# Performance work log

Measured on AMD Instinct MI355X. Metric: run time of the kernel, lower is better.

## Reference

```python
import jax, jax.numpy as jnp
import numpy as np

N = 100_000   # nodes
E = 3_200_000 # edges (avg degree 32)
F_NODE = 64
F_EDGE = 16
HID = 64
NEG_SLOPE = 0.2


def _gat_conv(x, src, dst, edge_attr, W, a_src, a_dst, We, a_e, bias, n):
    """PyG GATConv (heads=1, edge_dim, add_self_loops=True fill='mean', eval mode)."""
    # --- add self loops; loop edge_attr = mean of incoming edge_attr per node ---
    deg = jax.ops.segment_sum(jnp.ones((src.shape[0],), x.dtype), dst, num_segments=n)
    loop_attr = jax.ops.segment_sum(edge_attr, dst, num_segments=n)
    loop_attr = jnp.where(deg[:, None] > 0, loop_attr / jnp.maximum(deg, 1.0)[:, None], 0.0)
    loop = jnp.arange(n, dtype=src.dtype)
    src2 = jnp.concatenate([src, loop])
    dst2 = jnp.concatenate([dst, loop])
    ea = jnp.concatenate([edge_attr, loop_attr], axis=0)

    # --- node / edge projections and per-node attention terms ---
    h = x @ W                                   # [N, HID]
    alpha_src = h @ a_src                       # [N]
    alpha_dst = h @ a_dst                       # [N]
    e = ea @ We                                 # [E+N, HID]
    alpha_e = e @ a_e                           # [E+N]

    # --- per-edge logits + segment softmax over destination neighborhoods ---
    logits = jax.nn.leaky_relu(alpha_src[src2] + alpha_dst[dst2] + alpha_e, NEG_SLOPE)
    seg_max = jax.ops.segment_max(logits, dst2, num_segments=n)  # every node has self loop
    ex = jnp.exp(logits - seg_max[dst2])
    denom = jax.ops.segment_sum(ex, dst2, num_segments=n)
    w = ex / denom[dst2]                        # [E+N]

    # --- weighted scatter-aggregate of messages ---
    out = jax.ops.segment_sum(h[src2] * w[:, None], dst2, num_segments=n)
    return out + bias


def setup_inputs() -> dict:
    key = jax.random.key(0)
    ks = jax.random.split(key, 16)
    s = 0.1  # keep logits tame
    return {
        "x": jax.random.normal(ks[0], (N, F_NODE), jnp.float32),
        "edge_index": jax.random.randint(ks[1], (2, E), 0, N, jnp.int32),
        "edge_attr": jax.random.normal(ks[2], (E, F_EDGE), jnp.float32),
        "W1": jax.random.normal(ks[3], (F_NODE, HID), jnp.float32) * s,
        "att_src1": jax.random.normal(ks[4], (HID,), jnp.float32) * s,
        "att_dst1": jax.random.normal(ks[5], (HID,), jnp.float32) * s,
        "We1": jax.random.normal(ks[6], (F_EDGE, HID), jnp.float32) * s,
        "att_edge1": jax.random.normal(ks[7], (HID,), jnp.float32) * s,
        "b1": jnp.zeros((HID,), jnp.float32),
        "W2": jax.random.normal(ks[8], (HID, HID), jnp.float32) * s,
        "att_src2": jax.random.normal(ks[9], (HID,), jnp.float32) * s,
        "att_dst2": jax.random.normal(ks[10], (HID,), jnp.float32) * s,
        "We2": jax.random.normal(ks[11], (F_EDGE, HID), jnp.float32) * s,
        "att_edge2": jax.random.normal(ks[12], (HID,), jnp.float32) * s,
        "b2": jnp.zeros((HID,), jnp.float32),
        "fc_w": jax.random.normal(ks[13], (HID, 1), jnp.float32) * s,
        "fc_b": jnp.zeros((1,), jnp.float32),
    }


def reference(x, edge_index, edge_attr, W1, att_src1, att_dst1, We1, att_edge1, b1,
              W2, att_src2, att_dst2, We2, att_edge2, b2, fc_w, fc_b):
    src, dst = edge_index[0], edge_index[1]
    n = x.shape[0]
    h = jax.nn.elu(_gat_conv(x, src, dst, edge_attr, W1, att_src1, att_dst1, We1, att_edge1, b1, n))
    h = jax.nn.elu(_gat_conv(h, src, dst, edge_attr, W2, att_src2, att_dst2, We2, att_edge2, b2, n))
    return h @ fc_w + fc_b  # [N, 1] logits
```

## Files before the change

kernel.cpp:

```cpp
#include <hip/hip_runtime.h>
#include <hip/hip_bf16.h>
#include <hip/hip_fp16.h>
#include <math.h>
#include <stdint.h>

constexpr int HIDDIM = 64;
constexpr int FEDGE  = 16;
constexpr int BN     = 512;
constexpr int CAP    = 17000;
constexpr int TILE   = 4096;
constexpr int NTA    = 512;
constexpr int EPT    = TILE / NTA;

__global__ void compute_c_kernel(const float* __restrict__ We1, const float* __restrict__ ae1,
                                 const float* __restrict__ We2, const float* __restrict__ ae2,
                                 float* __restrict__ c) {
  int t = threadIdx.x;
  if (t < FEDGE) {
    float s = 0.f;
    for (int j = 0; j < HIDDIM; ++j) s += We1[t * HIDDIM + j] * ae1[j];
    c[t] = s;
  } else if (t < 2 * FEDGE) {
    int k = t - FEDGE;
    float s = 0.f;
    for (int j = 0; j < HIDDIM; ++j) s += We2[k * HIDDIM + j] * ae2[j];
    c[FEDGE + k] = s;
  }
}

__device__ __forceinline__ int pack_ae(float a1, float a2) {
  unsigned lo = __half_as_ushort(__float2half_rn(a1));
  unsigned hi = __half_as_ushort(__float2half_rn(a2));
  return (int)((hi << 16) | lo);
}
template <int SEL>
__device__ __forceinline__ float unpack_ae(int pk) {
  unsigned u = (SEL == 0) ? ((unsigned)pk & 0xFFFFu) : ((unsigned)pk >> 16);
  return __half2float(__ushort_as_half((unsigned short)u));
}

__global__ __launch_bounds__(NTA) void passA_kernel(
    const int* __restrict__ src, const int* __restrict__ dst,
    const float* __restrict__ attr, const float* __restrict__ c,
    int* __restrict__ bucketCursor, int2* __restrict__ P, int E, int nbuck) {
  __shared__ int st_ae[TILE];
  __shared__ int s_key[TILE];
  __shared__ int s_ae[TILE];
  __shared__ unsigned char s_b[TILE];
  __shared__ int cnt[256];
  __shared__ int lbase[512];
  __shared__ int gbase[256];
  __shared__ int wsum[8];
  __shared__ float cs[32];
  int t = threadIdx.x;
  if (t < 32) cs[t] = c[t];
  if (t < nbuck) cnt[t] = 0;
  __syncthreads();
  int e0 = blockIdx.x * TILE;
  int tileCnt = min(TILE, E - e0);

  int d_reg[EPT];
#pragma unroll
  for (int k = 0; k < EPT; ++k) {
    int e = e0 + k * NTA + t;
    d_reg[k] = (e < E) ? dst[e] : -1;
  }
#pragma unroll
  for (int k = 0; k < EPT; ++k) {
    if (d_reg[k] >= 0) atomicAdd(&cnt[d_reg[k] >> 9], 1);
  }
  __syncthreads();

  int lane = t & 63, w = t >> 6;
  int n = (t < nbuck) ? cnt[t] : 0;
  int ret = 0;
  if (n > 0) ret = atomicAdd(&bucketCursor[t], n);
  int incl = n;
#pragma unroll
  for (int d = 1; d < 64; d <<= 1) {
    int tv = __shfl_up(incl, d, 64);
    if (lane >= d) incl += tv;
  }
  if (lane == 63) wsum[w] = incl;
  __syncthreads();
  {
    int woff = 0;
#pragma unroll
    for (int w2 = 0; w2 < 8; ++w2) woff += (w2 < w) ? wsum[w2] : 0;
    lbase[t] = incl - n + woff;
    if (t < nbuck) { gbase[t] = ret; cnt[t] = 0; }
  }

  {
    int q   = t & 3;
    int grp = t >> 2;
    const float4* attr4 = (const float4*)attr;
#pragma unroll
    for (int pass = 0; pass < TILE / 128; ++pass) {
      int el = pass * 128 + grp;
      int e = e0 + el;
      float4 v = make_float4(0.f, 0.f, 0.f, 0.f);
      if (e < E) v = attr4[(size_t)e * 4 + q];
      float a1 = v.x * cs[4*q]    + v.y * cs[4*q+1]    + v.z * cs[4*q+2]    + v.w * cs[4*q+3];
      float a2 = v.x * cs[16+4*q] + v.y * cs[16+4*q+1] + v.z * cs[16+4*q+2] + v.w * cs[16+4*q+3];
      a1 += __shfl_xor(a1, 1, 64); a1 += __shfl_xor(a1, 2, 64);
      a2 += __shfl_xor(a2, 1, 64); a2 += __shfl_xor(a2, 2, 64);
      if (q == 0) st_ae[el] = pack_ae(a1, a2);
    }
  }
  __syncthreads();

#pragma unroll
  for (int k = 0; k < EPT; ++k) {
    int d = d_reg[k];
    if (d < 0) continue;
    int el = k * NTA + t;
    int e = e0 + el;
    int b = d >> 9;
    int sE = src[e];
    int r = atomicAdd(&cnt[b], 1);
    int idx = lbase[b] + r;
    s_key[idx] = sE | ((d & 511) << 20);
    s_ae[idx]  = st_ae[el];
    s_b[idx]   = (unsigned char)b;
  }
  __syncthreads();

  for (int i = t; i < tileCnt; i += NTA) {
    int b = s_b[i];
    int rank = i - lbase[b];
    int pos = gbase[b] + rank;
    if (pos < CAP) P[(size_t)b * CAP + pos] = make_int2(s_key[i], s_ae[i]);
  }
}

__global__ void scan_buckets_kernel(const int* __restrict__ bucketCursor,
                                    int* __restrict__ bucketBase,
                                    int* __restrict__ offsets, int nbuck, int N, int E) {
  __shared__ int s[512];
  int t = threadIdx.x;
  int v = (t < nbuck) ? min(bucketCursor[t], CAP) : 0;
  s[t] = v;
  __syncthreads();
  for (int d = 1; d < 512; d <<= 1) {
    int tv = (t >= d) ? s[t - d] : 0;
    __syncthreads();
    s[t] += tv;
    __syncthreads();
  }
  if (t < nbuck) bucketBase[t] = s[t] - v;
  if (t == 0) offsets[N] = E;
}

__global__ __launch_bounds__(512) void passB_kernel(
    const int2* __restrict__ P, const int* __restrict__ bucketCursor,
    const int* __restrict__ bucketBase, int* __restrict__ offsets,
    int2* __restrict__ EDGS, int N) {
  int b = blockIdx.x;
  int t = threadIdx.x;
  int nodeBase = b * BN;
  int cnt = min(bucketCursor[b], CAP);
  int gbase = bucketBase[b];
  __shared__ int hist[BN];
  __shared__ int cur[BN];
  __shared__ int wsum[8];
  hist[t] = 0;
  __syncthreads();
  const int2* Pb = P + (size_t)b * CAP;
  for (int i = t; i < cnt; i += 512) {
    int dl = (Pb[i].x >> 20) & 511;
    atomicAdd(&hist[dl], 1);
  }
  __syncthreads();
  int deg = hist[t];
  int lane = t & 63, w = t >> 6;
  int incl = deg;
#pragma unroll
  for (int d = 1; d < 64; d <<= 1) {
    int tv = __shfl_up(incl, d, 64);
    if (lane >= d) incl += tv;
  }
  if (lane == 63) wsum[w] = incl;
  __syncthreads();
  int woff = 0;
#pragma unroll
  for (int w2 = 0; w2 < 8; ++w2) woff += (w2 < w) ? wsum[w2] : 0;
  int excl = incl - deg + woff;
  int nodeId = nodeBase + t;
  if (nodeId < N) offsets[nodeId] = gbase + excl;
  cur[t] = gbase + excl;
  __syncthreads();
  for (int i = t; i < cnt; i += 512) {
    int2 r = Pb[i];
    int dl = (r.x >> 20) & 511;
    int pos = atomicAdd(&cur[dl], 1);
    EDGS[pos] = r;
  }
}

__global__ __launch_bounds__(256) void gemm_alpha_kernel(
    const float* __restrict__ X, const float* __restrict__ W,
    const float* __restrict__ a_src, const float* __restrict__ a_dst,
    __half2* __restrict__ H, float* __restrict__ alpha_s, float* __restrict__ alpha_d, int n) {
  __shared__ float Ws[HIDDIM * HIDDIM];
  __shared__ float as_s[HIDDIM], ad_s[HIDDIM];
  for (int i = threadIdx.x; i < HIDDIM * HIDDIM; i += blockDim.x) Ws[i] = W[i];
  if (threadIdx.x < HIDDIM) {
    as_s[threadIdx.x] = a_src[threadIdx.x];
    ad_s[threadIdx.x] = a_dst[threadIdx.x];
  }
  __syncthreads();
  int lane = threadIdx.x & 63;
  int wid  = threadIdx.x >> 6;
  int wavesTotal = (blockDim.x >> 6) * gridDim.x;
  for (int row = blockIdx.x * (blockDim.x >> 6) + wid; row < n; row += wavesTotal) {
    float xv = X[(size_t)row * HIDDIM + lane];
    float acc = 0.f;
#pragma unroll
    for (int k = 0; k < HIDDIM; ++k) {
      float xk = __shfl(xv, k, 64);
      acc = fmaf(xk, Ws[k * HIDDIM + lane], acc);
    }
    float accN = __shfl_xor(acc, 1, 64);
    if (!(lane & 1)) {
      H[(size_t)row * 32 + (lane >> 1)] = __floats2half2_rn(acc, accN);
    }
    float s1 = acc * as_s[lane];
    float s2 = acc * ad_s[lane];
#pragma unroll
    for (int d = 32; d > 0; d >>= 1) {
      s1 += __shfl_xor(s1, d, 64);
      s2 += __shfl_xor(s2, d, 64);
    }
    if (lane == 0) {
      alpha_s[row] = s1;
      alpha_d[row] = s2;
    }
  }
}

__device__ __forceinline__ float leaky(float x) { return (x < 0.f) ? 0.2f * x : x; }
__device__ __forceinline__ float elu(float x) { return (x > 0.f) ? x : (__expf(x) - 1.f); }

template <bool FINAL, int SEL>
__global__ __launch_bounds__(256) void aggregate_kernel(
    const __half2* __restrict__ H, const float* __restrict__ alpha_s, const float* __restrict__ alpha_d,
    const int2* __restrict__ EDGS, const int* __restrict__ offsets,
    const float* __restrict__ bias, const float* __restrict__ fc_w, const float* __restrict__ fc_b,
    float* __restrict__ out, int n) {
  int lane = threadIdx.x & 63;
  int wid  = threadIdx.x >> 6;
  int node = blockIdx.x * (blockDim.x >> 6) + wid;
  if (node >= n) return;
  int off = offsets[node];
  int deg = offsets[node + 1] - off;
  float ad  = alpha_d[node];
  float asn = alpha_s[node];

  if (deg <= 64) {
    int2 ed = make_int2(0, 0);
    if (lane < deg) ed = EDGS[off + lane];
    int   s_l  = ed.x & 0xFFFFF;
    float ae_l = unpack_ae<SEL>(ed.y);
    float as_g = (lane < deg) ? alpha_s[s_l] : 0.f;
    float lg_l = (lane < deg) ? leaky(as_g + ad + ae_l) : -INFINITY;
    float aesum = (lane < deg) ? ae_l : 0.f;
    float lmax = lg_l;
#pragma unroll
    for (int d = 32; d > 0; d >>= 1) {
      lmax = fmaxf(lmax, __shfl_xor(lmax, d, 64));
      aesum += __shfl_xor(aesum, d, 64);
    }
    float self_ae = (deg > 0) ? aesum / (float)deg : 0.f;
    float slg = leaky(asn + ad + self_ae);
    float m = fmaxf(lmax, slg);

    float ex_l = (lane < deg) ? __expf(lg_l - m) : 0.f;
    float dsum = ex_l;
#pragma unroll
    for (int d = 32; d > 0; d >>= 1) dsum += __shfl_xor(dsum, d, 64);
    float exs = __expf(slg - m);
    float denom = dsum + exs;

    int half = lane >> 5;
    int c32  = lane & 31;

    float selfw = (half == 0) ? exs : 0.f;
    float2 hv = __half22float2(H[(size_t)node * 32 + c32]);
    float2 acc2;
    acc2.x = selfw * hv.x;
    acc2.y = selfw * hv.y;

    int jj = 0;
    for (; jj + 16 <= deg; jj += 16) {
      int   si[8]; float ei[8];
#pragma unroll
      for (int k = 0; k < 8; ++k) {
        si[k] = __shfl(s_l, jj + 2 * k + half, 64);
        ei[k] = __shfl(ex_l, jj + 2 * k + half, 64);
      }
      float2 hh[8];
#pragma unroll
      for (int k = 0; k < 8; ++k) hh[k] = __half22float2(H[(size_t)si[k] * 32 + c32]);
#pragma unroll
      for (int k = 0; k < 8; ++k) {
        acc2.x = fmaf(ei[k], hh[k].x, acc2.x);
        acc2.y = fmaf(ei[k], hh[k].y, acc2.y);
      }
    }
    for (; jj + 8 <= deg; jj += 8) {
      int j0 = jj + half, j1 = jj + 2 + half, j2 = jj + 4 + half, j3 = jj + 6 + half;
      int   sa = __shfl(s_l, j0, 64),  sb = __shfl(s_l, j1, 64);
      int   sc = __shfl(s_l, j2, 64),  sd = __shfl(s_l, j3, 64);
      float ea = __shfl(ex_l, j0, 64), eb = __shfl(ex_l, j1, 64);
      float ec = __shfl(ex_l, j2, 64), ef = __shfl(ex_l, j3, 64);
      float2 ha = __half22float2(H[(size_t)sa * 32 + c32]);
      float2 hb = __half22float2(H[(size_t)sb * 32 + c32]);
      float2 hc = __half22float2(H[(size_t)sc * 32 + c32]);
      float2 hd = __half22float2(H[(size_t)sd * 32 + c32]);
      acc2.x = fmaf(ea, ha.x, acc2.x); acc2.y = fmaf(ea, ha.y, acc2.y);
      acc2.x = fmaf(eb, hb.x, acc2.x); acc2.y = fmaf(eb, hb.y, acc2.y);
      acc2.x = fmaf(ec, hc.x, acc2.x); acc2.y = fmaf(ec, hc.y, acc2.y);
      acc2.x = fmaf(ef, hd.x, acc2.x); acc2.y = fmaf(ef, hd.y, acc2.y);
    }
    for (; jj < deg; jj += 2) {
      int j = jj + half;
      int   sj = __shfl(s_l, j, 64);
      float ej = __shfl(ex_l, j, 64);
      float2 hj = __half22float2(H[(size_t)sj * 32 + c32]);
      acc2.x = fmaf(ej, hj.x, acc2.x);
      acc2.y = fmaf(ej, hj.y, acc2.y);
    }
    acc2.x += __shfl_xor(acc2.x, 32, 64);
    acc2.y += __shfl_xor(acc2.y, 32, 64);

    const float2* bi2 = (const float2*)bias;
    float2 bv = bi2[c32];
    float rx = elu(acc2.x / denom + bv.x);
    float ry = elu(acc2.y / denom + bv.y);
    if (!FINAL) {
      if (half == 0) {
        float2 o; o.x = rx; o.y = ry;
        ((float2*)out)[(size_t)node * 32 + c32] = o;
      }
    } else {
      const float2* fw2 = (const float2*)fc_w;
      float2 fv = fw2[c32];
      float s1 = rx * fv.x + ry * fv.y;
#pragma unroll
      for (int d = 16; d > 0; d >>= 1) s1 += __shfl_xor(s1, d, 64);
      if (lane == 0) out[node] = s1 + fc_b[0];
    }
    return;
  }

  {
    const __half* Hh = (const __half*)H;
    float lmax = -INFINITY, aesum = 0.f;
    for (int base = 0; base < deg; base += 64) {
      int i = base + lane;
      if (i < deg) {
        int2 ed = EDGS[off + i];
        int s = ed.x & 0xFFFFF;
        float ae = unpack_ae<SEL>(ed.y);
        float lg = leaky(alpha_s[s] + ad + ae);
        lmax = fmaxf(lmax, lg);
        aesum += ae;
      }
    }
#pragma unroll
    for (int d = 32; d > 0; d >>= 1) {
      lmax = fmaxf(lmax, __shfl_xor(lmax, d, 64));
      aesum += __shfl_xor(aesum, d, 64);
    }
    float self_ae = aesum / (float)deg;
    float slg = leaky(asn + ad + self_ae);
    float m = fmaxf(lmax, slg);
    float exs = __expf(slg - m);
    float dsum = 0.f;
    float acc = exs * __half2float(Hh[(size_t)node * HIDDIM + lane]);
    for (int base = 0; base < deg; base += 64) {
      int i = base + lane;
      int cnt = min(64, deg - base);
      int2 ed = make_int2(0, 0);
      if (i < deg) ed = EDGS[off + i];
      int   s_l  = ed.x & 0xFFFFF;
      float ae_l = unpack_ae<SEL>(ed.y);
      float ex_l = (lane < cnt) ? __expf(leaky(alpha_s[s_l] + ad + ae_l) - m) : 0.f;
      dsum += ex_l;
      for (int j = 0; j < cnt; ++j) {
        int   sj = __shfl(s_l, j, 64);
        float ej = __shfl(ex_l, j, 64);
        acc = fmaf(ej, __half2float(Hh[(size_t)sj * HIDDIM + lane]), acc);
      }
    }
#pragma unroll
    for (int d = 32; d > 0; d >>= 1) dsum += __shfl_xor(dsum, d, 64);
    float denom = dsum + exs;

    float res = elu(acc / denom + bias[lane]);
    if (!FINAL) {
      out[(size_t)node * HIDDIM + lane] = res;
    } else {
      float s1 = res * fc_w[lane];
#pragma unroll
      for (int d = 32; d > 0; d >>= 1) s1 += __shfl_xor(s1, d, 64);
      if (lane == 0) out[node] = s1 + fc_b[0];
    }
  }
}

extern "C" void kernel_launch(void* const* d_in, const int* in_sizes, int n_in,
                              void* d_out, int out_size, void* d_ws, size_t ws_size,
                              hipStream_t stream) {
  const float* x    = (const float*)d_in[0];
  const int*   ei   = (const int*)d_in[1];
  const float* attr = (const float*)d_in[2];
  const float* W1   = (const float*)d_in[3];
  const float* as1  = (const float*)d_in[4];
  const float* ad1  = (const float*)d_in[5];
  const float* We1  = (const float*)d_in[6];
  const float* ae1  = (const float*)d_in[7];
  const float* b1   = (const float*)d_in[8];
  const float* W2   = (const float*)d_in[9];
  const float* as2  = (const float*)d_in[10];
  const float* ad2  = (const float*)d_in[11];
  const float* We2  = (const float*)d_in[12];
  const float* ae2  = (const float*)d_in[13];
  const float* b2   = (const float*)d_in[14];
  const float* fcw  = (const float*)d_in[15];
  const float* fcb  = (const float*)d_in[16];

  const int N = in_sizes[0] / HIDDIM;
  const int E = in_sizes[1] / 2;
  const int NBUCK = (N + BN - 1) / BN;

  char* p = (char*)d_ws;
  auto alloc = [&](size_t bytes) -> void* {
    void* r = (void*)p;
    p += (bytes + 255) & ~(size_t)255;
    return r;
  };
  float*  c            = (float*)alloc(32 * sizeof(float));
  int*    bucketCursor = (int*)alloc(512 * 4);
  int*    bucketBase   = (int*)alloc(((size_t)NBUCK + 1) * 4);
  int*    offsets      = (int*)alloc(((size_t)N + 1) * 4);
  float*  alpha_s      = (float*)alloc((size_t)N * 4);
  float*  alpha_d      = (float*)alloc((size_t)N * 4);
  int2*   EDGS         = (int2*)alloc((size_t)E * 8);
  size_t  regionBytes  = (size_t)NBUCK * CAP * 8;
  size_t  hBytes       = (size_t)N * HIDDIM * 2;
  size_t  x2Bytes      = (size_t)N * HIDDIM * 4;
  if (hBytes + x2Bytes > regionBytes) regionBytes = hBytes + x2Bytes;
  char*   region       = (char*)alloc(regionBytes);
  int2*   P            = (int2*)region;
  __half2* H           = (__half2*)region;
  float*  X2           = (float*)(region + ((hBytes + 255) & ~(size_t)255));

  const int* srcp = ei;
  const int* dstp = ei + E;

  hipMemsetAsync(bucketCursor, 0, 512 * 4, stream);

  compute_c_kernel<<<1, 64, 0, stream>>>(We1, ae1, We2, ae2, c);

  int ablocks = (E + TILE - 1) / TILE;
  passA_kernel<<<ablocks, NTA, 0, stream>>>(srcp, dstp, attr, c, bucketCursor, P, E, NBUCK);
  scan_buckets_kernel<<<1, 512, 0, stream>>>(bucketCursor, bucketBase, offsets, NBUCK, N, E);
  passB_kernel<<<NBUCK, 512, 0, stream>>>(P, bucketCursor, bucketBase, offsets, EDGS, N);

  int aggBlocks = (N + 3) / 4;

  gemm_alpha_kernel<<<2048, 256, 0, stream>>>(x, W1, as1, ad1, H, alpha_s, alpha_d, N);
  aggregate_kernel<false, 0><<<aggBlocks, 256, 0, stream>>>(H, alpha_s, alpha_d, EDGS,
                                                            offsets, b1, nullptr, nullptr, X2, N);
  gemm_alpha_kernel<<<2048, 256, 0, stream>>>(X2, W2, as2, ad2, H, alpha_s, alpha_d, N);
  aggregate_kernel<true, 1><<<aggBlocks, 256, 0, stream>>>(H, alpha_s, alpha_d, EDGS,
                                                           offsets, b2, fcw, fcb, (float*)d_out, N);
}
```

Before: 447.2 us.

## Fuse layer-1 aggregation with layer-2 projection and attention terms

Adds a kernel that performs the layer-1 softmax aggregation, bias and ELU, then immediately multiplies the result by W2 (held in shared memory) and computes the layer-2 alpha_src/alpha_dst terms per node. This removes the fp32 X2 intermediate write and read and one kernel launch. The cost is extra shared-memory use, a 64-step shuffle-based matvec per node, and a persistent grid-stride loop. New buffers H2 and alpha_s2/alpha_d2 avoid overwriting layer-1 data that other waves are still reading.

```diff
diff --git a/kernel.cpp b/kernel.cpp
--- a/kernel.cpp
+++ b/kernel.cpp
@@ -241,6 +241,169 @@
 
 __device__ __forceinline__ float leaky(float x) { return (x < 0.f) ? 0.2f * x : x; }
 __device__ __forceinline__ float elu(float x) { return (x > 0.f) ? x : (__expf(x) - 1.f); }
+
+__global__ __launch_bounds__(256) void agg_gemm_kernel(
+    const __half2* __restrict__ H, const float* __restrict__ alpha_s, const float* __restrict__ alpha_d,
+    const int2* __restrict__ EDGS, const int* __restrict__ offsets,
+    const float* __restrict__ bias, const float* __restrict__ W2,
+    const float* __restrict__ as2, const float* __restrict__ ad2,
+    __half2* __restrict__ H2, float* __restrict__ alpha_s2, float* __restrict__ alpha_d2, int n) {
+  __shared__ float W2s[HIDDIM * HIDDIM];
+  __shared__ float as2s[HIDDIM], ad2s[HIDDIM];
+  for (int i = threadIdx.x; i < HIDDIM * HIDDIM; i += 256) W2s[i] = W2[i];
+  if (threadIdx.x < HIDDIM) {
+    as2s[threadIdx.x] = as2[threadIdx.x];
+    ad2s[threadIdx.x] = ad2[threadIdx.x];
+  }
+  __syncthreads();
+  int lane = threadIdx.x & 63;
+  int wid  = threadIdx.x >> 6;
+  int wavesTotal = 4 * gridDim.x;
+  int half = lane >> 5;
+  int c32  = lane & 31;
+
+  for (int node = blockIdx.x * 4 + wid; node < n; node += wavesTotal) {
+    int off = offsets[node];
+    int deg = offsets[node + 1] - off;
+    float ad  = alpha_d[node];
+    float asn = alpha_s[node];
+    float rx, ry;
+
+    if (deg <= 64) {
+      int2 ed = make_int2(0, 0);
+      if (lane < deg) ed = EDGS[off + lane];
+      int   s_l  = ed.x & 0xFFFFF;
+      float ae_l = unpack_ae<0>(ed.y);
+      float as_g = (lane < deg) ? alpha_s[s_l] : 0.f;
+      float lg_l = (lane < deg) ? leaky(as_g + ad + ae_l) : -INFINITY;
+      float aesum = (lane < deg) ? ae_l : 0.f;
+      float lmax = lg_l;
+#pragma unroll
+      for (int d = 32; d > 0; d >>= 1) {
+        lmax = fmaxf(lmax, __shfl_xor(lmax, d, 64));
+        aesum += __shfl_xor(aesum, d, 64);
+      }
+      float self_ae = (deg > 0) ? aesum / (float)deg : 0.f;
+      float slg = leaky(asn + ad + self_ae);
+      float m = fmaxf(lmax, slg);
+      float ex_l = (lane < deg) ? __expf(lg_l - m) : 0.f;
+      float dsum = ex_l;
+#pragma unroll
+      for (int d = 32; d > 0; d >>= 1) dsum += __shfl_xor(dsum, d, 64);
+      float exs = __expf(slg - m);
+      float denom = dsum + exs;
+
+      float selfw = (half == 0) ? exs : 0.f;
+      float2 hv = __half22float2(H[(size_t)node * 32 + c32]);
+      float2 acc2;
+      acc2.x = selfw * hv.x;
+      acc2.y = selfw * hv.y;
+
+      int jj = 0;
+      for (; jj + 16 <= deg; jj += 16) {
+        int   si[8]; float ei[8];
+#pragma unroll
+        for (int k = 0; k < 8; ++k) {
+          si[k] = __shfl(s_l, jj + 2 * k + half, 64);
+          ei[k] = __shfl(ex_l, jj + 2 * k + half, 64);
+        }
+        float2 hh[8];
+#pragma unroll
+        for (int k = 0; k < 8; ++k) hh[k] = __half22float2(H[(size_t)si[k] * 32 + c32]);
+#pragma unroll
+        for (int k = 0; k < 8; ++k) {
+          acc2.x = fmaf(ei[k], hh[k].x, acc2.x);
+          acc2.y = fmaf(ei[k], hh[k].y, acc2.y);
+        }
+      }
+      for (; jj < deg; jj += 2) {
+        int j = jj + half;
+        int   sj = __shfl(s_l, j, 64);
+        float ej = __shfl(ex_l, j, 64);
+        float2 hj = __half22float2(H[(size_t)sj * 32 + c32]);
+        acc2.x = fmaf(ej, hj.x, acc2.x);
+        acc2.y = fmaf(ej, hj.y, acc2.y);
+      }
+      acc2.x += __shfl_xor(acc2.x, 32, 64);
+      acc2.y += __shfl_xor(acc2.y, 32, 64);
+
+      const float2* bi2 = (const float2*)bias;
+      float2 bv = bi2[c32];
+      rx = elu(acc2.x / denom + bv.x);
+      ry = elu(acc2.y / denom + bv.y);
+    } else {
+      const __half* Hh = (const __half*)H;
+      float lmax = -INFINITY, aesum = 0.f;
+      for (int base = 0; base < deg; base += 64) {
+        int i = base + lane;
+        if (i < deg) {
+          int2 ed = EDGS[off + i];
+          int s = ed.x & 0xFFFFF;
+          float ae = unpack_ae<0>(ed.y);
+          float lg = leaky(alpha_s[s] + ad + ae);
+          lmax = fmaxf(lmax, lg);
+          aesum += ae;
+        }
+      }
+#pragma unroll
+      for (int d = 32; d > 0; d >>= 1) {
+        lmax = fmaxf(lmax, __shfl_xor(lmax, d, 64));
+        aesum += __shfl_xor(aesum, d, 64);
+      }
+      float self_ae = aesum / (float)deg;
+      float slg = leaky(asn + ad + self_ae);
+      float m = fmaxf(lmax, slg);
+      float exs = __expf(slg - m);
+      float dsum = 0.f;
+      float acc = exs * __half2float(Hh[(size_t)node * HIDDIM + lane]);
+      for (int base = 0; base < deg; base += 64) {
+        int i = base + lane;
+        int cnt = min(64, deg - base);
+        int2 ed = make_int2(0, 0);
+        if (i < deg) ed = EDGS[off + i];
+        int   s_l  = ed.x & 0xFFFFF;
+        float ae_l = unpack_ae<0>(ed.y);
+        float ex_l = (lane < cnt) ? __expf(leaky(alpha_s[s_l] + ad + ae_l) - m) : 0.f;
+        dsum += ex_l;
+        for (int j = 0; j < cnt; ++j) {
+          int   sj = __shfl(s_l, j, 64);
+          float ej = __shfl(ex_l, j, 64);
+          acc = fmaf(ej, __half2float(Hh[(size_t)sj * HIDDIM + lane]), acc);
+        }
+      }
+#pragma unroll
+      for (int d = 32; d > 0; d >>= 1) dsum += __shfl_xor(dsum, d, 64);
+      float denom = dsum + exs;
+      float res = elu(acc / denom + bias[lane]);
+      rx = __shfl(res, 2 * c32, 64);
+      ry = __shfl(res, 2 * c32 + 1, 64);
+    }
+
+    float h2 = 0.f;
+#pragma unroll
+    for (int cc = 0; cc < 32; ++cc) {
+      float r0 = __shfl(rx, cc, 64);
+      float r1 = __shfl(ry, cc, 64);
+      h2 = fmaf(r0, W2s[(2 * cc) * HIDDIM + lane], h2);
+      h2 = fmaf(r1, W2s[(2 * cc + 1) * HIDDIM + lane], h2);
+    }
+    float h2N = __shfl_xor(h2, 1, 64);
+    if (!(lane & 1)) {
+      H2[(size_t)node * 32 + (lane >> 1)] = __floats2half2_rn(h2, h2N);
+    }
+    float s1 = h2 * as2s[lane];
+    float s2 = h2 * ad2s[lane];
+#pragma unroll
+    for (int d = 32; d > 0; d >>= 1) {
+      s1 += __shfl_xor(s1, d, 64);
+      s2 += __shfl_xor(s2, d, 64);
+    }
+    if (lane == 0) {
+      alpha_s2[node] = s1;
+      alpha_d2[node] = s2;
+    }
+  }
+}
 
 template <bool FINAL, int SEL>
 __global__ __launch_bounds__(256) void aggregate_kernel(
@@ -447,15 +610,16 @@
   int*    offsets      = (int*)alloc(((size_t)N + 1) * 4);
   float*  alpha_s      = (float*)alloc((size_t)N * 4);
   float*  alpha_d      = (float*)alloc((size_t)N * 4);
+  float*  alpha_s2     = (float*)alloc((size_t)N * 4);
+  float*  alpha_d2     = (float*)alloc((size_t)N * 4);
   int2*   EDGS         = (int2*)alloc((size_t)E * 8);
+  __half2* H2          = (__half2*)alloc((size_t)N * 32 * 4);
   size_t  regionBytes  = (size_t)NBUCK * CAP * 8;
   size_t  hBytes       = (size_t)N * HIDDIM * 2;
-  size_t  x2Bytes      = (size_t)N * HIDDIM * 4;
-  if (hBytes + x2Bytes > regionBytes) regionBytes = hBytes + x2Bytes;
+  if (hBytes > regionBytes) regionBytes = hBytes;
   char*   region       = (char*)alloc(regionBytes);
   int2*   P            = (int2*)region;
-  __half2* H           = (__half2*)region;
-  float*  X2           = (float*)(region + ((hBytes + 255) & ~(size_t)255));
+  __half2* H1          = (__half2*)region;
 
   const int* srcp = ei;
   const int* dstp = ei + E;
@@ -469,12 +633,12 @@
   scan_buckets_kernel<<<1, 512, 0, stream>>>(bucketCursor, bucketBase, offsets, NBUCK, N, E);
   passB_kernel<<<NBUCK, 512, 0, stream>>>(P, bucketCursor, bucketBase, offsets, EDGS, N);
 
+  gemm_alpha_kernel<<<2048, 256, 0, stream>>>(x, W1, as1, ad1, H1, alpha_s, alpha_d, N);
+
+  agg_gemm_kernel<<<2048, 256, 0, stream>>>(H1, alpha_s, alpha_d, EDGS, offsets, b1,
+                                            W2, as2, ad2, H2, alpha_s2, alpha_d2, N);
+
   int aggBlocks = (N + 3) / 4;
-
-  gemm_alpha_kernel<<<2048, 256, 0, stream>>>(x, W1, as1, ad1, H, alpha_s, alpha_d, N);
-  aggregate_kernel<false, 0><<<aggBlocks, 256, 0, stream>>>(H, alpha_s, alpha_d, EDGS,
-                                                            offsets, b1, nullptr, nullptr, X2, N);
-  gemm_alpha_kernel<<<2048, 256, 0, stream>>>(X2, W2, as2, ad2, H, alpha_s, alpha_d, N);
-  aggregate_kernel<true, 1><<<aggBlocks, 256, 0, stream>>>(H, alpha_s, alpha_d, EDGS,
+  aggregate_kernel<true, 1><<<aggBlocks, 256, 0, stream>>>(H2, alpha_s2, alpha_d2, EDGS,
                                                            offsets, b2, fcw, fcb, (float*)d_out, N);
 }
```

Result: slower. 492.7 us (+10.2%).
